# Optimization experiments

Measured on AMD Instinct MI355X. Metric: run time of the kernel, lower is better.

The kernel has to match this reference:

```python
import jax, jax.numpy as jnp
import numpy as np

B, N1, N2, K, D, C_IN = 2, 8192, 8192, 16, 64, 131
MLP = [128, 128]
WN_HID = [8, 8]


def _sqdist(src, dst):
    # src [B,N,3], dst [B,M,3] -> [B,N,M], clamped at 0 like the torch code
    d = (jnp.sum(src * src, -1)[:, :, None]
         + jnp.sum(dst * dst, -1)[:, None, :]
         - 2.0 * jnp.einsum('bnc,bmc->bnm', src, dst))
    return jnp.maximum(d, 0.0)


def _knn(k, xyz, query):
    # k smallest distances (torch.topk largest=False)
    _, idx = jax.lax.top_k(-_sqdist(query, xyz), k)
    return idx  # [B,S,k]


def _gather(points, idx):
    # points [B,N,C], idx [B,S,K] -> [B,S,K,C]
    return jax.vmap(lambda p, i: p[i])(points, idx)


def _mlp(x, Ws, bs, act):
    # x [B,N,K,Cin]; 1x1 Conv2d == per-point linear
    for W, b in zip(Ws, bs):
        x = act(jnp.einsum('bnkc,oc->bnko', x, W) + b)
    return x


_leaky = lambda x: jax.nn.leaky_relu(x, 0.1)
_relu = jax.nn.relu


def setup_inputs() -> dict:
    key = jax.random.key(0)
    ks = iter(jax.random.split(key, 32))

    def conv(cout, cin):
        s = 1.0 / np.sqrt(cin)
        w = jax.random.uniform(next(ks), (cout, cin), jnp.float32, -s, s)
        b = jax.random.uniform(next(ks), (cout,), jnp.float32, -s, s)
        return w, b

    inp = {
        'pc1': jax.random.normal(next(ks), (B, 3, N1), jnp.float32),
        'pc2': jax.random.normal(next(ks), (B, 3, N2), jnp.float32),
        'feature1': jax.random.normal(next(ks), (B, D, N1), jnp.float32),
        'feature2': jax.random.normal(next(ks), (B, D, N2), jnp.float32),
    }
    # main mlp convs: 131 -> 128 -> 128
    c = C_IN
    for i, co in enumerate(MLP):
        inp[f'mlp_W{i}'], inp[f'mlp_b{i}'] = conv(co, c)
        c = co
    # weightnet1/2: 3 -> 8 -> 8 -> 128
    for name in ('wn1', 'wn2'):
        dims = [3] + WN_HID + [MLP[-1]]
        for i in range(len(dims) - 1):
            inp[f'{name}_W{i}'], inp[f'{name}_b{i}'] = conv(dims[i + 1], dims[i])
    return inp


def reference(pc1, pc2, feature1, feature2,
              mlp_W0, mlp_b0, mlp_W1, mlp_b1,
              wn1_W0, wn1_b0, wn1_W1, wn1_b1, wn1_W2, wn1_b2,
              wn2_W0, wn2_b0, wn2_W1, wn2_b1, wn2_W2, wn2_b2):
    nsample = K
    p1 = pc1.transpose(0, 2, 1)    # [B,N1,3]
    p2 = pc2.transpose(0, 2, 1)    # [B,N2,3]
    f1 = feature1.transpose(0, 2, 1)  # [B,N1,D1]
    f2 = feature2.transpose(0, 2, 1)  # [B,N2,D2]
    b, n1, _ = p1.shape

    # cross-cloud KNN grouping
    idx = _knn(nsample, p2, p1)                 # [B,N1,K]
    direction_xyz = _gather(p2, idx) - p1[:, :, None, :]   # [B,N1,K,3]
    gf2 = _gather(f2, idx)                      # [B,N1,K,D2]
    gf1 = jnp.broadcast_to(f1[:, :, None, :], (b, n1, nsample, f1.shape[-1]))
    new_features = jnp.concatenate([gf1, gf2, direction_xyz], -1)  # [B,N1,K,131]

    new_features = _mlp(new_features, [mlp_W0, mlp_W1], [mlp_b0, mlp_b1], _leaky)
    weights = _mlp(direction_xyz, [wn1_W0, wn1_W1, wn1_W2],
                   [wn1_b0, wn1_b1, wn1_b2], _relu)
    new_features = jnp.sum(weights * new_features, axis=2)  # [B,N1,Cout]

    # self KNN re-aggregation
    idx2 = _knn(nsample, p1, p1)
    dir2 = _gather(p1, idx2) - p1[:, :, None, :]
    weights2 = _mlp(dir2, [wn2_W0, wn2_W1, wn2_W2],
                    [wn2_b0, wn2_b1, wn2_b2], _relu)
    grouped = _gather(new_features, idx2)        # [B,N1,K,Cout]
    out = jnp.sum(weights2 * grouped, axis=2)    # [B,N1,Cout]
    return out.transpose(0, 2, 1)                # [B,Cout,N1]
```

## Files before the change

### kernel.cpp

```cpp
#include <hip/hip_runtime.h>

typedef __attribute__((ext_vector_type(8))) short short8;
typedef __attribute__((ext_vector_type(4))) float f32x4;

#define NPTS 8192
#define NB 2
#define KNN 16
#define KP 20
#define LDX 168
#define LDH 136

__device__ inline ushort f2bf(float x){
  unsigned u = __float_as_uint(x);
  return (ushort)((u + 0x7FFFu + ((u >> 16) & 1u)) >> 16);
}
__device__ inline float leaky(float x){ return x > 0.f ? x : 0.1f * x; }
__device__ inline f32x4 mfma16(short8 a, short8 b, f32x4 c){
  return __builtin_amdgcn_mfma_f32_16x16x32_bf16(a, b, c, 0, 0, 0);
}
__device__ inline int cellkey(float x, float y, float z){
  int ix = (int)((x + 3.f) * (16.f / 6.f));
  int iy = (int)((y + 3.f) * (16.f / 6.f));
  int iz = (int)((z + 3.f) * (16.f / 6.f));
  ix = ix < 0 ? 0 : (ix > 15 ? 15 : ix);
  iy = iy < 0 ? 0 : (iy > 15 ? 15 : iy);
  iz = iz < 0 ? 0 : (iz > 15 ? 15 : iz);
  int key = 0;
  #pragma unroll
  for (int i = 0; i < 4; ++i)
    key |= (((ix >> i) & 1) << (3 * i + 2)) | (((iy >> i) & 1) << (3 * i + 1)) | (((iz >> i) & 1) << (3 * i));
  return key;
}

__global__ __launch_bounds__(256) void k_misc(const float* __restrict__ pc1, const float* __restrict__ pc2,
                                              float4* __restrict__ p1, float4* __restrict__ p2,
                                              const float* __restrict__ W0, const float* __restrict__ W1,
                                              ushort* __restrict__ W0p, ushort* __restrict__ W1p){
  int bid = blockIdx.x;
  if (bid < 64){
    int i = bid * 256 + threadIdx.x;
    int b = i >> 13, n = i & (NPTS - 1);
    const float* s1 = pc1 + (size_t)b * 3 * NPTS + n;
    const float* s2 = pc2 + (size_t)b * 3 * NPTS + n;
    p1[i] = make_float4(s1[0], s1[NPTS], s1[2 * NPTS], 0.f);
    p2[i] = make_float4(s2[0], s2[NPTS], s2[2 * NPTS], 0.f);
  } else if (bid == 64){
    for (int e = threadIdx.x; e < 8 * 5 * 64 * 8; e += 256){
      int i = e & 7, ln = (e >> 3) & 63, t = e >> 9, kt = t % 5, ct = t / 5;
      int col = ct * 16 + (ln & 15), k = kt * 32 + 8 * (ln >> 4) + i;
      W0p[e] = f2bf(k < 131 ? W0[col * 131 + k] : 0.f);
    }
  } else {
    for (int e = threadIdx.x; e < 8 * 4 * 64 * 8; e += 256){
      int i = e & 7, ln = (e >> 3) & 63, t = e >> 9, kt = t & 3, ct = t >> 2;
      int col = ct * 16 + (ln & 15), k = kt * 32 + 8 * (ln >> 4) + i;
      W1p[e] = f2bf(W1[col * 128 + k]);
    }
  }
}

__global__ __launch_bounds__(256) void k_transpose(const float* __restrict__ f1, const float* __restrict__ f2,
                                                   ushort* __restrict__ o1, ushort* __restrict__ o2){
  __shared__ ushort tile[64][257];
  int bid = blockIdx.x;
  int feat = bid >> 6; int b = (bid >> 5) & 1; int n0 = (bid & 31) * 256;
  const float* src = (feat ? f2 : f1) + (size_t)b * 64 * NPTS;
  ushort* dst = (feat ? o2 : o1) + (size_t)b * NPTS * 64;
  for (int rep = 0; rep < 64; ++rep){
    int lin = rep * 256 + threadIdx.x;
    int j = lin >> 8, nn = lin & 255;
    tile[j][nn] = f2bf(src[(size_t)j * NPTS + n0 + nn]);
  }
  __syncthreads();
  for (int rep = 0; rep < 64; ++rep){
    int lin = rep * 256 + threadIdx.x;
    int nn = lin >> 6, j = lin & 63;
    dst[(size_t)(n0 + nn) * 64 + j] = tile[j][nn];
  }
}

__global__ __launch_bounds__(1024) void k_sort(const float4* __restrict__ p1, const float4* __restrict__ p2,
                                               float4* __restrict__ sp1, float4* __restrict__ sp2,
                                               int* __restrict__ cs1, int* __restrict__ cs2){
  __shared__ int hist[4096];
  __shared__ int tsum[1024];
  int bid = blockIdx.x;
  int b = bid >> 1, cloud = bid & 1;
  const float4* src = (cloud ? p2 : p1) + b * NPTS;
  float4* dst = (cloud ? sp2 : sp1) + b * NPTS;
  int* cs = (cloud ? cs2 : cs1) + b * 4100;
  int tid = threadIdx.x;
  #pragma unroll
  for (int i = 0; i < 4; ++i) hist[tid + i * 1024] = 0;
  __syncthreads();
  int keys[8];
  #pragma unroll
  for (int i = 0; i < 8; ++i){
    float4 v = src[i * 1024 + tid];
    keys[i] = cellkey(v.x, v.y, v.z);
    atomicAdd(&hist[keys[i]], 1);
  }
  __syncthreads();
  int h[4], s = 0;
  #pragma unroll
  for (int i = 0; i < 4; ++i){ h[i] = hist[tid * 4 + i]; s += h[i]; }
  tsum[tid] = s;
  __syncthreads();
  for (int off = 1; off < 1024; off <<= 1){
    int v = tsum[tid];
    if (tid >= off) v += tsum[tid - off];
    __syncthreads();
    tsum[tid] = v;
    __syncthreads();
  }
  int ex = tid ? tsum[tid - 1] : 0;
  #pragma unroll
  for (int i = 0; i < 4; ++i){ int c = h[i]; hist[tid * 4 + i] = ex; cs[tid * 4 + i] = ex; ex += c; }
  if (tid == 1023) cs[4096] = NPTS;
  __syncthreads();
  #pragma unroll
  for (int i = 0; i < 8; ++i){
    float4 v = src[i * 1024 + tid];
    int pos = atomicAdd(&hist[keys[i]], 1);
    dst[pos] = make_float4(v.x, v.y, v.z, __int_as_float(i * 1024 + tid));
  }
}

__global__ __launch_bounds__(256) void k_knn(const float4* __restrict__ p1,
                                             const float4* __restrict__ sp1, const float4* __restrict__ sp2,
                                             const int* __restrict__ cs1, const int* __restrict__ cs2,
                                             int* __restrict__ idx1, int* __restrict__ idx2){
  __shared__ float sx[1024], sy[1024], sz[1024];
  int tid = threadIdx.x, lane = tid & 63, wv = tid >> 6;
  int bid = blockIdx.x;
  int task = bid >> 10, rem = bid & 1023;
  int b = rem >> 9; int q0 = (rem & 511) * 16;
  const float4* __restrict__ cpb = (task ? sp1 : sp2) + b * NPTS;
  const int* __restrict__ cs = (task ? cs1 : cs2) + b * 4100;
  int* __restrict__ outIdx = task ? idx2 : idx1;
  int qbase = b * NPTS + q0 + wv * 4;
  float qx[4], qy[4], qz[4], sd[4], thr[4]; int si[4];
  #pragma unroll
  for (int i = 0; i < 4; ++i){
    float4 qq = p1[qbase + i];
    qx[i] = qq.x; qy[i] = qq.y; qz[i] = qq.z;
  }
  #pragma unroll
  for (int q = 0; q < 4; ++q){
    int key = cellkey(qx[q], qy[q], qz[q]);
    int st = cs[key], en = cs[key + 1];
    int wstart = st + ((en - st) >> 1) - 128;
    wstart = wstart < 0 ? 0 : (wstart > NPTS - 256 ? NPTS - 256 : wstart);
    float mn = 1e30f;
    #pragma unroll
    for (int i = 0; i < 4; ++i){
      float4 c = cpb[wstart + i * 64 + lane];
      float dx = c.x - qx[q], dy = c.y - qy[q], dz = c.z - qz[q];
      mn = fminf(mn, fmaf(dx, dx, fmaf(dy, dy, dz * dz)));
    }
    float v = mn;
    #pragma unroll
    for (int k = 2; k <= 64; k <<= 1){
      #pragma unroll
      for (int j = k >> 1; j > 0; j >>= 1){
        float o = __shfl_xor(v, j);
        bool asc = ((lane & k) == 0);
        bool upper = ((lane & j) != 0);
        v = (asc != upper) ? fminf(v, o) : fmaxf(v, o);
      }
    }
    float t0 = __shfl(v, KP - 1);
    thr[q] = __uint_as_float(__float_as_uint(t0) + 1u);
    sd[q] = 1e30f; si[q] = 0;
  }
  for (int ch = 0; ch < 8; ++ch){
    __syncthreads();
    for (int t = tid; t < 1024; t += 256){
      float4 cc = cpb[ch * 1024 + t];
      sx[t] = cc.x; sy[t] = cc.y; sz[t] = cc.z;
    }
    __syncthreads();
    for (int it = 0; it < 16; ++it){
      float cx = sx[it * 64 + lane], cy = sy[it * 64 + lane], cz = sz[it * 64 + lane];
      int jb = ch * 1024 + it * 64;
      #pragma unroll
      for (int q = 0; q < 4; ++q){
        float dx = cx - qx[q], dy = cy - qy[q], dz = cz - qz[q];
        float d = fmaf(dx, dx, fmaf(dy, dy, dz * dz));
        unsigned long long m = __ballot(d < thr[q]);
        while (m){
          int src = __ffsll((unsigned long long)m) - 1;
          m &= m - 1;
          float dv = __shfl(d, src);
          if (dv >= thr[q]) continue;
          int iv = jb + src;
          float ud = __shfl_up(sd[q], 1);
          int   ui = __shfl_up(si[q], 1);
          int pos = __popcll(__ballot(sd[q] <= dv) & 0xFFFFFull);
          bool lt = lane < pos;
          bool eq = lane == pos;
          float nd = lt ? sd[q] : (eq ? dv : ud);
          int   ni = lt ? si[q] : (eq ? iv : ui);
          sd[q] = nd; si[q] = ni;
          thr[q] = fminf(thr[q], __shfl(nd, KP - 1));
        }
      }
    }
  }
  #pragma unroll
  for (int q = 0; q < 4; ++q){
    double dd = -1.0;
    int myi = si[q];
    int orig = 0;
    if (lane < KP){
      float4 cc = cpb[myi];
      orig = __float_as_int(cc.w);
      double dx = (double)cc.x - (double)qx[q];
      double dy = (double)cc.y - (double)qy[q];
      double dz = (double)cc.z - (double)qz[q];
      dd = dx * dx + dy * dy + dz * dz;
    }
    #pragma unroll
    for (int rep = 0; rep < 4; ++rep){
      double mx = dd; int mi = lane;
      #pragma unroll
      for (int off = 32; off; off >>= 1){
        double om = __shfl_xor(mx, off);
        int oi = __shfl_xor(mi, off);
        if (om > mx || (om == mx && oi < mi)){ mx = om; mi = oi; }
      }
      if (lane == mi) dd = -1.0;
    }
    unsigned long long keep = __ballot(dd >= 0.0);
    int rank = __popcll(keep & ((1ull << lane) - 1ull));
    if (dd >= 0.0) outIdx[(size_t)(b * NPTS + q0 + wv * 4 + q) * KNN + rank] = orig;
  }
}

__global__ __launch_bounds__(256) void k_fused(
    const float4* __restrict__ p1, const float4* __restrict__ p2,
    const ushort* __restrict__ f1b, const ushort* __restrict__ f2b,
    const int* __restrict__ idx1,
    const ushort* __restrict__ W0p, const ushort* __restrict__ W1p,
    const float* __restrict__ b0, const float* __restrict__ b1,
    const float* __restrict__ wn1W0, const float* __restrict__ wn1b0,
    const float* __restrict__ wn1W1, const float* __restrict__ wn1b1,
    const float* __restrict__ wn1W2, const float* __restrict__ wn1b2,
    float* __restrict__ NF)
{
  __shared__ ushort Xs[128 * LDX];
  __shared__ float dirS[128][4];
  __shared__ float h2S[128][8];
  __shared__ float W2s[128][8];
  __shared__ float b0S[128], b1S[128], b2S[128];
  __shared__ int idxS[128];
  int tid = threadIdx.x, lane = tid & 63, wv = tid >> 6;
  int bid = blockIdx.x;
  int b = bid >> 10; int n0 = (bid & 1023) << 3;
  int base = b * NPTS;
  for (int t = tid; t < 1024; t += 256) ((float*)W2s)[t] = wn1W2[t];
  if (tid < 128){
    b0S[tid] = b0[tid]; b1S[tid] = b1[tid]; b2S[tid] = wn1b2[tid];
    int p = tid >> 4;
    int id = idx1[(size_t)(base + n0 + p) * KNN + (tid & 15)];
    idxS[tid] = id;
    float4 c = p2[base + id];
    float4 q = p1[base + n0 + p];
    float dx = c.x - q.x, dy = c.y - q.y, dz = c.z - q.z;
    dirS[tid][0] = dx; dirS[tid][1] = dy; dirS[tid][2] = dz; dirS[tid][3] = 0.f;
    ushort* xr = Xs + tid * LDX;
    xr[128] = f2bf(dx); xr[129] = f2bf(dy); xr[130] = f2bf(dz);
    #pragma unroll
    for (int j = 131; j < 160; ++j) xr[j] = 0;
  }
  __syncthreads();
  {
    int r = tid >> 1, hf = tid & 1;
    const uint4* s = (const uint4*)(hf ? (f2b + (size_t)(base + idxS[r]) * 64)
                                       : (f1b + (size_t)(base + n0 + (r >> 4)) * 64));
    uint4* d = (uint4*)(Xs + r * LDX + hf * 64);
    #pragma unroll
    for (int j = 0; j < 8; ++j) d[j] = s[j];
  }
  __syncthreads();
  int r0 = wv * 32;
  f32x4 zero4 = {0.f, 0.f, 0.f, 0.f};
  f32x4 acc[2][8];
  #pragma unroll
  for (int mt = 0; mt < 2; ++mt)
    #pragma unroll
    for (int ct = 0; ct < 8; ++ct) acc[mt][ct] = zero4;
  #pragma unroll
  for (int kt = 0; kt < 5; ++kt){
    const ushort* ab = Xs + (r0 + (lane & 15)) * LDX + kt * 32 + 8 * (lane >> 4);
    short8 a0 = *(const short8*)ab;
    short8 a1 = *(const short8*)(ab + 16 * LDX);
    #pragma unroll
    for (int ct = 0; ct < 8; ++ct){
      short8 bb = *(const short8*)(W0p + (size_t)((ct * 5 + kt) * 64 + lane) * 8);
      acc[0][ct] = mfma16(a0, bb, acc[0][ct]);
      acc[1][ct] = mfma16(a1, bb, acc[1][ct]);
    }
  }
  __syncthreads();
  ushort* Hs = Xs;
  #pragma unroll
  for (int mt = 0; mt < 2; ++mt)
    #pragma unroll
    for (int ct = 0; ct < 8; ++ct){
      int col = ct * 16 + (lane & 15);
      float bb = b0S[col];
      #pragma unroll
      for (int r = 0; r < 4; ++r){
        int row = r0 + mt * 16 + 4 * (lane >> 4) + r;
        Hs[row * LDH + col] = f2bf(leaky(acc[mt][ct][r] + bb));
      }
    }
  if (tid < 128){
    float d0 = dirS[tid][0], d1 = dirS[tid][1], d2 = dirS[tid][2];
    float h1[8];
    #pragma unroll
    for (int i = 0; i < 8; ++i)
      h1[i] = fmaxf(fmaf(wn1W0[i * 3 + 2], d2, fmaf(wn1W0[i * 3 + 1], d1, fmaf(wn1W0[i * 3], d0, wn1b0[i]))), 0.f);
    #pragma unroll
    for (int i = 0; i < 8; ++i){
      float s = wn1b1[i];
      #pragma unroll
      for (int j = 0; j < 8; ++j) s = fmaf(wn1W1[i * 8 + j], h1[j], s);
      h2S[tid][i] = fmaxf(s, 0.f);
    }
  }
  __syncthreads();
  #pragma unroll
  for (int mt = 0; mt < 2; ++mt)
    #pragma unroll
    for (int ct = 0; ct < 8; ++ct) acc[mt][ct] = zero4;
  #pragma unroll
  for (int kt = 0; kt < 4; ++kt){
    const ushort* ab = Hs + (r0 + (lane & 15)) * LDH + kt * 32 + 8 * (lane >> 4);
    short8 a0 = *(const short8*)ab;
    short8 a1 = *(const short8*)(ab + 16 * LDH);
    #pragma unroll
    for (int ct = 0; ct < 8; ++ct){
      short8 bb = *(const short8*)(W1p + (size_t)((ct * 4 + kt) * 64 + lane) * 8);
      acc[0][ct] = mfma16(a0, bb, acc[0][ct]);
      acc[1][ct] = mfma16(a1, bb, acc[1][ct]);
    }
  }
  #pragma unroll
  for (int ct = 0; ct < 8; ++ct){
    int col = ct * 16 + (lane & 15);
    float4 w2a = *(const float4*)&W2s[col][0];
    float4 w2b = *(const float4*)&W2s[col][4];
    float bw = b2S[col], bg = b1S[col];
    #pragma unroll
    for (int mt = 0; mt < 2; ++mt){
      float s = 0.f;
      #pragma unroll
      for (int r = 0; r < 4; ++r){
        int row = r0 + mt * 16 + 4 * (lane >> 4) + r;
        const float4 ha = *(const float4*)&h2S[row][0];
        const float4 hb = *(const float4*)&h2S[row][4];
        float w = bw;
        w = fmaf(w2a.x, ha.x, w); w = fmaf(w2a.y, ha.y, w); w = fmaf(w2a.z, ha.z, w); w = fmaf(w2a.w, ha.w, w);
        w = fmaf(w2b.x, hb.x, w); w = fmaf(w2b.y, hb.y, w); w = fmaf(w2b.z, hb.z, w); w = fmaf(w2b.w, hb.w, w);
        w = fmaxf(w, 0.f);
        float g = leaky(acc[mt][ct][r] + bg);
        s = fmaf(w, g, s);
      }
      s += __shfl_xor(s, 16);
      s += __shfl_xor(s, 32);
      if (lane < 16) NF[(size_t)(base + n0 + wv * 2 + mt) * 128 + col] = s;
    }
  }
}

__global__ __launch_bounds__(256) void k_reagg(
    const float4* __restrict__ p1, const int* __restrict__ idx2,
    const float* __restrict__ NF,
    const float* __restrict__ wn2W0, const float* __restrict__ wn2b0,
    const float* __restrict__ wn2W1, const float* __restrict__ wn2b1,
    const float* __restrict__ wn2W2, const float* __restrict__ wn2b2,
    float* __restrict__ out)
{
  __shared__ float h2L[4][16][8];
  __shared__ int idxL[4][16];
  __shared__ float outT[128][20];
  int tid = threadIdx.x, lane = tid & 63, wv = tid >> 6;
  int bid = blockIdx.x;
  int b = bid >> 9; int n0 = (bid & 511) * 16;
  int base = b * NPTS;
  for (int pp = 0; pp < 4; ++pp){
    int np = wv * 4 + pp;
    int n = n0 + np;
    if (lane < 16){
      int id = idx2[(size_t)(base + n) * KNN + lane];
      idxL[wv][lane] = id;
      float4 c = p1[base + id];
      float4 q = p1[base + n];
      float d0 = c.x - q.x, d1 = c.y - q.y, d2 = c.z - q.z;
      float h1[8];
      #pragma unroll
      for (int i = 0; i < 8; ++i)
        h1[i] = fmaxf(fmaf(wn2W0[i * 3 + 2], d2, fmaf(wn2W0[i * 3 + 1], d1, fmaf(wn2W0[i * 3], d0, wn2b0[i]))), 0.f);
      #pragma unroll
      for (int i = 0; i < 8; ++i){
        float s = wn2b1[i];
        #pragma unroll
        for (int j = 0; j < 8; ++j) s = fmaf(wn2W1[i * 8 + j], h1[j], s);
        h2L[wv][lane][i] = fmaxf(s, 0.f);
      }
    }
    __syncthreads();
    #pragma unroll
    for (int hf = 0; hf < 2; ++hf){
      int c = hf * 64 + lane;
      float4 w2a = *(const float4*)(wn2W2 + c * 8);
      float4 w2b = *(const float4*)(wn2W2 + c * 8 + 4);
      float accv = 0.f, bw = wn2b2[c];
      #pragma unroll
      for (int k = 0; k < 16; ++k){
        const float4 ha = *(const float4*)&h2L[wv][k][0];
        const float4 hb = *(const float4*)&h2L[wv][k][4];
        float w = bw;
        w = fmaf(w2a.x, ha.x, w); w = fmaf(w2a.y, ha.y, w); w = fmaf(w2a.z, ha.z, w); w = fmaf(w2a.w, ha.w, w);
        w = fmaf(w2b.x, hb.x, w); w = fmaf(w2b.y, hb.y, w); w = fmaf(w2b.z, hb.z, w); w = fmaf(w2b.w, hb.w, w);
        w = fmaxf(w, 0.f);
        float g = NF[(size_t)(base + idxL[wv][k]) * 128 + c];
        accv = fmaf(w, g, accv);
      }
      outT[c][np] = accv;
    }
    __syncthreads();
  }
  {
    int c = tid >> 1, jh = (tid & 1) * 8;
    float4 v0 = *(const float4*)&outT[c][jh];
    float4 v1 = *(const float4*)&outT[c][jh + 4];
    size_t ob = ((size_t)b * 128 + c) * NPTS + n0 + jh;
    *(float4*)(out + ob) = v0;
    *(float4*)(out + ob + 4) = v1;
  }
}

extern "C" void kernel_launch(void* const* d_in, const int* in_sizes, int n_in,
                              void* d_out, int out_size, void* d_ws, size_t ws_size,
                              hipStream_t stream)
{
  const float* pc1 = (const float*)d_in[0];
  const float* pc2 = (const float*)d_in[1];
  const float* f1  = (const float*)d_in[2];
  const float* f2  = (const float*)d_in[3];
  const float* mW0 = (const float*)d_in[4];
  const float* mb0 = (const float*)d_in[5];
  const float* mW1 = (const float*)d_in[6];
  const float* mb1 = (const float*)d_in[7];
  const float* w1W0 = (const float*)d_in[8];
  const float* w1b0 = (const float*)d_in[9];
  const float* w1W1 = (const float*)d_in[10];
  const float* w1b1 = (const float*)d_in[11];
  const float* w1W2 = (const float*)d_in[12];
  const float* w1b2 = (const float*)d_in[13];
  const float* w2W0 = (const float*)d_in[14];
  const float* w2b0 = (const float*)d_in[15];
  const float* w2W1 = (const float*)d_in[16];
  const float* w2b1 = (const float*)d_in[17];
  const float* w2W2 = (const float*)d_in[18];
  const float* w2b2 = (const float*)d_in[19];

  char* ws = (char*)d_ws;
  float4* p1f4 = (float4*)(ws + 0);
  float4* p2f4 = (float4*)(ws + 262144);
  ushort* f1b  = (ushort*)(ws + 524288);
  ushort* f2b  = (ushort*)(ws + 2621440);
  int* idx1    = (int*)(ws + 4718592);
  int* idx2    = (int*)(ws + 6815744);
  ushort* W0p  = (ushort*)(ws + 8912896);
  ushort* W1p  = (ushort*)(ws + 8953856);
  float* NF    = (float*)(ws + 8986624);
  float4* sp1  = (float4*)(ws + 8986624);
  float4* sp2  = (float4*)(ws + 9248768);
  int* cs1     = (int*)(ws + 9510912);
  int* cs2     = (int*)(ws + 9543712);
  float* out   = (float*)d_out;

  hipLaunchKernelGGL(k_misc, dim3(66), dim3(256), 0, stream, pc1, pc2, p1f4, p2f4, mW0, mW1, W0p, W1p);
  hipLaunchKernelGGL(k_sort, dim3(4), dim3(1024), 0, stream, p1f4, p2f4, sp1, sp2, cs1, cs2);
  hipLaunchKernelGGL(k_transpose, dim3(128), dim3(256), 0, stream, f1, f2, f1b, f2b);
  hipLaunchKernelGGL(k_knn, dim3(2048), dim3(256), 0, stream, p1f4, sp1, sp2, cs1, cs2, idx1, idx2);
  hipLaunchKernelGGL(k_fused, dim3(2048), dim3(256), 0, stream, p1f4, p2f4, f1b, f2b, idx1,
                     W0p, W1p, mb0, mb1, w1W0, w1b0, w1W1, w1b1, w1W2, w1b2, NF);
  hipLaunchKernelGGL(k_reagg, dim3(1024), dim3(256), 0, stream, p1f4, idx2, NF,
                     w2W0, w2b0, w2W1, w2b1, w2W2, w2b2, out);
}
```

Baseline: 348.7 us.

## Replace per-candidate wave insertion sort with threshold filtering into LDS buffer

The KNN scan no longer keeps a sorted top-20 list updated by a serial wave-wide insertion for every passing candidate. It ballots candidates under a fixed threshold (loosened slightly), compacts their indices into a per-query LDS buffer of up to 128 entries, and then picks the 16 nearest in double precision with 16 wave-reduction rounds. If more than 128 candidates pass, it falls back to a full rescan with the old insertion method. This removes the serialized while-loop from the hot scan. In exchange it adds LDS use, which may reduce occupancy, and a slow fallback path when the threshold is loose.

Measured after the change: 409.5 us. 17.4% more time.

```diff
diff --git a/kernel.cpp b/kernel.cpp
--- a/kernel.cpp
+++ b/kernel.cpp
@@ -7,6 +7,7 @@
 #define NB 2
 #define KNN 16
 #define KP 20
+#define CAP 128
 #define LDX 168
 #define LDH 136
 
@@ -131,6 +132,7 @@
                                              const int* __restrict__ cs1, const int* __restrict__ cs2,
                                              int* __restrict__ idx1, int* __restrict__ idx2){
   __shared__ float sx[1024], sy[1024], sz[1024];
+  __shared__ int bufS[4][4][CAP];
   int tid = threadIdx.x, lane = tid & 63, wv = tid >> 6;
   int bid = blockIdx.x;
   int task = bid >> 10, rem = bid & 1023;
@@ -139,7 +141,7 @@
   const int* __restrict__ cs = (task ? cs1 : cs2) + b * 4100;
   int* __restrict__ outIdx = task ? idx2 : idx1;
   int qbase = b * NPTS + q0 + wv * 4;
-  float qx[4], qy[4], qz[4], sd[4], thr[4]; int si[4];
+  float qx[4], qy[4], qz[4], thr[4]; int cnt[4];
   #pragma unroll
   for (int i = 0; i < 4; ++i){
     float4 qq = p1[qbase + i];
@@ -170,8 +172,8 @@
       }
     }
     float t0 = __shfl(v, KP - 1);
-    thr[q] = __uint_as_float(__float_as_uint(t0) + 1u);
-    sd[q] = 1e30f; si[q] = 0;
+    thr[q] = __uint_as_float(__float_as_uint(t0) + 8u);
+    cnt[q] = 0;
   }
   for (int ch = 0; ch < 8; ++ch){
     __syncthreads();
@@ -187,53 +189,104 @@
       for (int q = 0; q < 4; ++q){
         float dx = cx - qx[q], dy = cy - qy[q], dz = cz - qz[q];
         float d = fmaf(dx, dx, fmaf(dy, dy, dz * dz));
-        unsigned long long m = __ballot(d < thr[q]);
+        bool pass = d < thr[q];
+        unsigned long long m = __ballot(pass);
+        if (m){
+          int pre = __popcll(m & ((1ull << lane) - 1ull));
+          int pos = cnt[q] + pre;
+          if (pass && pos < CAP) bufS[wv][q][pos] = jb + lane;
+          cnt[q] += __popcll(m);
+        }
+      }
+    }
+  }
+  #pragma unroll 1
+  for (int q = 0; q < 4; ++q){
+    size_t orow = (size_t)(b * NPTS + q0 + wv * 4 + q) * KNN;
+    if (cnt[q] <= CAP){
+      int T = cnt[q];
+      double d0 = 1e300, d1 = 1e300; int o0 = 0, o1 = 0;
+      if (lane < T){
+        float4 c = cpb[bufS[wv][q][lane]];
+        o0 = __float_as_int(c.w);
+        double dx = (double)c.x - (double)qx[q];
+        double dy = (double)c.y - (double)qy[q];
+        double dz = (double)c.z - (double)qz[q];
+        d0 = dx * dx + dy * dy + dz * dz;
+      }
+      if (lane + 64 < T){
+        float4 c = cpb[bufS[wv][q][lane + 64]];
+        o1 = __float_as_int(c.w);
+        double dx = (double)c.x - (double)qx[q];
+        double dy = (double)c.y - (double)qy[q];
+        double dz = (double)c.z - (double)qz[q];
+        d1 = dx * dx + dy * dy + dz * dz;
+      }
+      int myOut = 0;
+      for (int r = 0; r < KNN; ++r){
+        double bd; int bp;
+        if (d0 <= d1){ bd = d0; bp = lane; } else { bd = d1; bp = lane | 64; }
+        #pragma unroll
+        for (int off = 32; off; off >>= 1){
+          double od = __shfl_xor(bd, off);
+          int op = __shfl_xor(bp, off);
+          if (od < bd || (od == bd && op < bp)){ bd = od; bp = op; }
+        }
+        if (lane == (bp & 63)){ if (bp & 64) d1 = 1e300; else d0 = 1e300; }
+        int cand = (bp & 64) ? o1 : o0;
+        int orig = __shfl(cand, bp & 63);
+        if (lane == r) myOut = orig;
+      }
+      if (lane < KNN) outIdx[orow + lane] = myOut;
+    } else {
+      float sdq = 1e30f; int siq = 0; float th = thr[q];
+      for (int t = lane; t < NPTS; t += 64){
+        int base0 = t - lane;
+        float4 c = cpb[t];
+        float dx = c.x - qx[q], dy = c.y - qy[q], dz = c.z - qz[q];
+        float d = fmaf(dx, dx, fmaf(dy, dy, dz * dz));
+        unsigned long long m = __ballot(d < th);
         while (m){
           int src = __ffsll((unsigned long long)m) - 1;
           m &= m - 1;
           float dv = __shfl(d, src);
-          if (dv >= thr[q]) continue;
-          int iv = jb + src;
-          float ud = __shfl_up(sd[q], 1);
-          int   ui = __shfl_up(si[q], 1);
-          int pos = __popcll(__ballot(sd[q] <= dv) & 0xFFFFFull);
+          if (dv >= th) continue;
+          int iv = base0 + src;
+          float ud = __shfl_up(sdq, 1);
+          int   ui = __shfl_up(siq, 1);
+          int pos = __popcll(__ballot(sdq <= dv) & 0xFFFFFull);
           bool lt = lane < pos;
           bool eq = lane == pos;
-          float nd = lt ? sd[q] : (eq ? dv : ud);
-          int   ni = lt ? si[q] : (eq ? iv : ui);
-          sd[q] = nd; si[q] = ni;
-          thr[q] = fminf(thr[q], __shfl(nd, KP - 1));
+          float nd = lt ? sdq : (eq ? dv : ud);
+          int   ni = lt ? siq : (eq ? iv : ui);
+          sdq = nd; siq = ni;
+          th = fminf(th, __shfl(nd, KP - 1));
         }
       }
-    }
-  }
-  #pragma unroll
-  for (int q = 0; q < 4; ++q){
-    double dd = -1.0;
-    int myi = si[q];
-    int orig = 0;
-    if (lane < KP){
-      float4 cc = cpb[myi];
-      orig = __float_as_int(cc.w);
-      double dx = (double)cc.x - (double)qx[q];
-      double dy = (double)cc.y - (double)qy[q];
-      double dz = (double)cc.z - (double)qz[q];
-      dd = dx * dx + dy * dy + dz * dz;
-    }
-    #pragma unroll
-    for (int rep = 0; rep < 4; ++rep){
-      double mx = dd; int mi = lane;
-      #pragma unroll
-      for (int off = 32; off; off >>= 1){
-        double om = __shfl_xor(mx, off);
-        int oi = __shfl_xor(mi, off);
-        if (om > mx || (om == mx && oi < mi)){ mx = om; mi = oi; }
-      }
-      if (lane == mi) dd = -1.0;
-    }
-    unsigned long long keep = __ballot(dd >= 0.0);
-    int rank = __popcll(keep & ((1ull << lane) - 1ull));
-    if (dd >= 0.0) outIdx[(size_t)(b * NPTS + q0 + wv * 4 + q) * KNN + rank] = orig;
+      double dd = -1.0; int orig = 0;
+      if (lane < KP){
+        float4 cc = cpb[siq];
+        orig = __float_as_int(cc.w);
+        double dx = (double)cc.x - (double)qx[q];
+        double dy = (double)cc.y - (double)qy[q];
+        double dz = (double)cc.z - (double)qz[q];
+        dd = dx * dx + dy * dy + dz * dz;
+      }
+      #pragma unroll
+      for (int rep = 0; rep < 4; ++rep){
+        double mx = dd; int mi = lane;
+        #pragma unroll
+        for (int off = 32; off; off >>= 1){
+          double om = __shfl_xor(mx, off);
+          int oi = __shfl_xor(mi, off);
+          if (om > mx || (om == mx && oi < mi)){ mx = om; mi = oi; }
+        }
+        if (lane == mi) dd = -1.0;
+      }
+      unsigned long long keep = __ballot(dd >= 0.0);
+      int rank = __popcll(keep & ((1ull << lane) - 1ull));
+      if (dd >= 0.0) outIdx[orow + rank] = orig;
+    }
   }
 }
 
```
